# Performance work log

Measured on AMD Instinct MI355X. Metric: run time of the kernel, lower is better.

## Reference

```python
import jax, jax.numpy as jnp
import numpy as np

N_POINTS = 400000
N_SEG = 4096


def setup_inputs() -> dict:
    key = jax.random.key(0)
    ks = jax.random.split(key, 8)
    inp = {
        "features": jax.random.normal(ks[0], (N_POINTS, 11), dtype=jnp.float32),
        "super_indices": jax.random.randint(ks[1], (N_POINTS,), 0, N_SEG, dtype=jnp.int64) if jax.config.jax_enable_x64 else jax.random.randint(ks[1], (N_POINTS,), 0, N_SEG).astype(jnp.int32),
        "num_segments": N_SEG,
        "W1": jax.random.normal(ks[2], (11, 128), dtype=jnp.float32) * 0.02,
        "b1": jnp.zeros((128,), jnp.float32),
        "W2": jax.random.normal(ks[3], (128, 256), dtype=jnp.float32) * 0.02,
        "b2": jnp.zeros((256,), jnp.float32),
        "W3": jax.random.normal(ks[4], (512, 512), dtype=jnp.float32) * 0.02,
        "b3": jnp.zeros((512,), jnp.float32),
        "W4": jax.random.normal(ks[5], (512, 384), dtype=jnp.float32) * 0.02,
        "b4": jnp.zeros((384,), jnp.float32),
    }
    return inp


def reference(features, super_indices, num_segments, W1, b1, W2, b2, W3, b3, W4, b4):
    # first_conv: two 1x1 Conv1d == per-point linears (no activation between, as in source)
    h = features @ W1 + b1            # [N,128]
    h = h @ W2 + b2                   # [N,256]
    # per-superpoint global max (torch.max over group points)
    g = jax.ops.segment_max(h, super_indices, num_segments=num_segments)  # [S,256]
    # concat broadcasted group-global with local features -> 512 channels
    hcat = jnp.concatenate([g[super_indices], h], axis=-1)                # [N,512]
    # second_conv: Conv1d(512,512,1) -> ReLU -> Conv1d(512,token_embed_dim,1)
    z = jax.nn.relu(hcat @ W3 + b3)   # [N,512]
    z = z @ W4 + b4                   # [N,384]
    # final per-superpoint max pool -> one token per superpoint
    sp_features = jax.ops.segment_max(z, super_indices, num_segments=num_segments)  # [S,384]
    return sp_features
```

## Files before the change

### kernel.cpp

```cpp
#include <hip/hip_runtime.h>
#include <stdint.h>

#define GAS __attribute__((address_space(1)))
#define LAS __attribute__((address_space(3)))

typedef unsigned short u16;
typedef short short8 __attribute__((ext_vector_type(8)));
typedef __bf16 bf16x8 __attribute__((ext_vector_type(8)));
typedef float floatx4 __attribute__((ext_vector_type(4)));

__device__ __forceinline__ u16 f2bf(float f) {
  uint32_t u = __builtin_bit_cast(uint32_t, f);
  u += 0x7FFFu + ((u >> 16) & 1u);
  return (u16)(u >> 16);
}
__device__ __forceinline__ float bf2f(u16 h) {
  return __builtin_bit_cast(float, (uint32_t)h << 16);
}
__device__ __forceinline__ void split_bf(float v, u16& hi, u16& lo) {
  hi = f2bf(v);
  float r = v - bf2f(hi);
  if (!(r == r)) r = 0.f;
  lo = f2bf(r);
}

__device__ __forceinline__ void atomicMaxF(float* addr, float val) {
  if (!(val > *(volatile const float*)addr)) return;
  if (val >= 0.f) atomicMax((int*)addr, __builtin_bit_cast(int, val));
  else            atomicMin((unsigned int*)addr, __builtin_bit_cast(unsigned int, val));
}

__device__ __forceinline__ void async16(const void* g, const void* lds) {
  __builtin_amdgcn_global_load_lds((GAS const uint32_t*)g, (LAS uint32_t*)lds, 16, 0, 0);
}

__device__ __forceinline__ floatx4 mfma_bf16(short8 a, short8 b, floatx4 c) {
  return __builtin_amdgcn_mfma_f32_16x16x32_bf16(
      __builtin_bit_cast(bf16x8, a), __builtin_bit_cast(bf16x8, b), c, 0, 0, 0);
}

__global__ void k_init(float* __restrict__ g, float* __restrict__ out,
                       int* __restrict__ hist, int ng, int no, int nh) {
  int i = blockIdx.x * 256 + threadIdx.x;
  if (i < ng) g[i] = -INFINITY;
  else if (i < ng + no) out[i - ng] = -INFINITY;
  else if (i < ng + no + nh) hist[i - ng - no] = 0;
}

__global__ void k_hist(const int* __restrict__ idx, int* __restrict__ hist, int n) {
  int p = blockIdx.x * 256 + threadIdx.x;
  if (p < n) atomicAdd(&hist[idx[p]], 1);
}

__global__ __launch_bounds__(1024) void k_scan(const int* __restrict__ hist,
                                               int* __restrict__ offs, int* __restrict__ cur) {
  __shared__ int buf[2][1024];
  int t = threadIdx.x;
  int local[4];
  int s = 0;
#pragma unroll
  for (int j = 0; j < 4; ++j) { local[j] = hist[t * 4 + j]; s += local[j]; }
  buf[0][t] = s;
  __syncthreads();
  int pb = 0;
  for (int d = 1; d < 1024; d <<= 1) {
    int v = buf[pb][t] + (t >= d ? buf[pb][t - d] : 0);
    buf[pb ^ 1][t] = v;
    pb ^= 1;
    __syncthreads();
  }
  int run = (t == 0) ? 0 : buf[pb][t - 1];
#pragma unroll
  for (int j = 0; j < 4; ++j) { offs[t * 4 + j] = run; cur[t * 4 + j] = run; run += local[j]; }
}

__global__ void k_scatter(const int* __restrict__ idx, int* __restrict__ cur,
                          int* __restrict__ perm, int* __restrict__ segp, int n) {
  int p = blockIdx.x * 256 + threadIdx.x;
  if (p >= n) return;
  int s = idx[p];
  int r = atomicAdd(&cur[s], 1);
  perm[r] = p;
  segp[r] = s;
}

__global__ void k_h1(const float* __restrict__ feat, const int* __restrict__ perm,
                     const float* __restrict__ W1, const float* __restrict__ b1,
                     u16* __restrict__ h1hi, u16* __restrict__ h1lo,
                     int pt_off, int npts_chunk) {
  int gid = blockIdx.x * 256 + threadIdx.x;
  int p = gid >> 7, c = gid & 127;
  if (p >= npts_chunk) return;
  int o = perm[pt_off + p];
  float v = b1[c];
#pragma unroll
  for (int j = 0; j < 11; ++j) v += feat[o * 11 + j] * W1[j * 128 + c];
  u16 hi, lo; split_bf(v, hi, lo);
  h1hi[gid] = hi; h1lo[gid] = lo;
}

__global__ void k_wprep(const float* __restrict__ W, u16* __restrict__ bt, int K, int N) {
  int gid = blockIdx.x * 256 + threadIdx.x;
  if (gid >= K * N) return;
  int c = gid / K, k = gid - c * K;
  float v = W[(size_t)k * N + c];
  u16 hi, lo; split_bf(v, hi, lo);
  size_t b = (size_t)c * (3 * K);
  bt[b + k] = hi; bt[b + K + k] = lo; bt[b + 2 * K + k] = hi;
}

__global__ void k_w23(const float* __restrict__ W2, const float* __restrict__ W3,
                      const float* __restrict__ b2, const float* __restrict__ b3,
                      float* __restrict__ W23, float* __restrict__ b23) {
  int gid = blockIdx.x * 256 + threadIdx.x;
  if (gid < 128 * 512) {
    int j = gid >> 9, c = gid & 511;
    float s = 0.f;
#pragma unroll 4
    for (int t = 0; t < 256; ++t) s += W2[j * 256 + t] * W3[(size_t)(256 + t) * 512 + c];
    W23[gid] = s;
  } else if (gid < 128 * 512 + 512) {
    int c = gid - 128 * 512;
    float s = b3[c];
    for (int t = 0; t < 256; ++t) s += b2[t] * W3[(size_t)(256 + t) * 512 + c];
    b23[c] = s;
  }
}

__global__ void k_prep3(const float* __restrict__ W3, const float* __restrict__ W23,
                        u16* __restrict__ bt) {
  int gid = blockIdx.x * 256 + threadIdx.x;
  if (gid >= 512 * 384) return;
  int c = gid / 384, k = gid - c * 384;
  float v = (k < 256) ? W3[(size_t)k * 512 + c] : W23[(size_t)(k - 256) * 512 + c];
  u16 hi, lo; split_bf(v, hi, lo);
  size_t b = (size_t)c * 1152;
  bt[b + k] = hi; bt[b + 384 + k] = lo; bt[b + 768 + k] = hi;
}

__global__ void k_gsplit(const float* __restrict__ g, u16* __restrict__ ghi,
                         u16* __restrict__ glo, int n) {
  int i = blockIdx.x * 256 + threadIdx.x;
  if (i >= n) return;
  u16 hi, lo; split_bf(g[i], hi, lo);
  ghi[i] = hi; glo[i] = lo;
}

template <int MODE, int KP, int NT, int CW>
__global__ __launch_bounds__(256) void k_gemm(
    const u16* __restrict__ a0, const u16* __restrict__ a1,
    const u16* __restrict__ a2, const u16* __restrict__ a3,
    const u16* __restrict__ bt, const float* __restrict__ bias,
    const int* __restrict__ segp, int mt0,
    float* __restrict__ gmax, u16* __restrict__ whi, u16* __restrict__ wlo) {
  __shared__ __align__(16) union {
    struct { u16 A[128 * 64]; u16 B[128 * 64]; } st;
    float ct[128 * 66];
  } sm;
  const int tid = threadIdx.x;
  const int w = tid >> 6, lane = tid & 63;
  const int mtl = blockIdx.x / NT, ct = blockIdx.x % NT;
  const int wr = w & 1, wc = w >> 1;
  const int l15 = lane & 15, l4 = lane >> 4;
  const int sub = lane >> 3;
  const int kc8 = (lane & 7) * 8;

  int arl[4], bcol[4], gq[4];
#pragma unroll
  for (int q = 0; q < 4; ++q) {
    int rr = (q * 4 + w) * 8 + sub;
    arl[q] = mtl * 128 + rr;
    bcol[q] = ct * 128 + rr;
    if constexpr (MODE == 1) gq[q] = segp[(mt0 + mtl) * 128 + rr];
  }

  floatx4 zero = {0.f, 0.f, 0.f, 0.f};
  floatx4 acc[4][4];
#pragma unroll
  for (int mi = 0; mi < 4; ++mi)
#pragma unroll
    for (int ni = 0; ni < 4; ++ni) acc[mi][ni] = zero;

  for (int kt = 0; kt < KP / 64; ++kt) {
    const int kbase = kt * 64 + kc8;
#pragma unroll
    for (int q = 0; q < 4; ++q) {
      const u16* src;
      if constexpr (MODE == 0) {
        int r = kbase >> 7, k = kbase & 127;
        src = ((r == 2) ? a1 : a0) + (size_t)arl[q] * 128 + k;
      } else if constexpr (MODE == 1) {
        int r = kbase / 384, inner = kbase - r * 384;
        bool lo = (r == 2);
        if (inner < 256) src = (lo ? a2 : a0) + (size_t)gq[q] * 256 + inner;
        else             src = (lo ? a3 : a1) + (size_t)arl[q] * 128 + (inner - 256);
      } else {
        int r = kbase >> 9, inner = kbase & 511;
        src = ((r == 2) ? a1 : a0) + (size_t)arl[q] * 512 + inner;
      }
      async16(src, &sm.st.A[(q * 4 + w) * 512]);
    }
#pragma unroll
    for (int q = 0; q < 4; ++q)
      async16(bt + (size_t)bcol[q] * KP + kbase, &sm.st.B[(q * 4 + w) * 512]);
    __syncthreads();
#pragma unroll
    for (int kk = 0; kk < 2; ++kk) {
      short8 af[4], bfr[4];
#pragma unroll
      for (int mi = 0; mi < 4; ++mi)
        af[mi] = *(const short8*)&sm.st.A[(wr * 64 + mi * 16 + l15) * 64 + kk * 32 + l4 * 8];
#pragma unroll
      for (int ni = 0; ni < 4; ++ni)
        bfr[ni] = *(const short8*)&sm.st.B[(wc * 64 + ni * 16 + l15) * 64 + kk * 32 + l4 * 8];
#pragma unroll
      for (int mi = 0; mi < 4; ++mi)
#pragma unroll
        for (int ni = 0; ni < 4; ++ni)
          acc[mi][ni] = mfma_bf16(af[mi], bfr[ni], acc[mi][ni]);
    }
    __syncthreads();
  }

  if constexpr (MODE == 1) {
#pragma unroll
    for (int ni = 0; ni < 4; ++ni) {
      const int col = ct * 128 + wc * 64 + ni * 16 + l15;
      const float bv = bias[col];
#pragma unroll
      for (int mi = 0; mi < 4; ++mi) {
        const int rl0 = mtl * 128 + wr * 64 + mi * 16 + l4 * 4;
#pragma unroll
        for (int r = 0; r < 4; ++r) {
          float v = fmaxf(acc[mi][ni][r] + bv, 0.f);
          u16 hi, lo; split_bf(v, hi, lo);
          whi[(size_t)(rl0 + r) * 512 + col] = hi;
          wlo[(size_t)(rl0 + r) * 512 + col] = lo;
        }
      }
    }
  } else {
#pragma unroll
    for (int h = 0; h < 2; ++h) {
      __syncthreads();
      if (wc == h) {
#pragma unroll
        for (int ni = 0; ni < 4; ++ni) {
          const int cl = ni * 16 + l15;
          const float bv = bias[ct * 128 + h * 64 + cl];
#pragma unroll
          for (int mi = 0; mi < 4; ++mi) {
            const int row0 = wr * 64 + mi * 16 + l4 * 4;
#pragma unroll
            for (int r = 0; r < 4; ++r)
              sm.ct[(row0 + r) * 66 + cl] = acc[mi][ni][r] + bv;
          }
        }
      }
      __syncthreads();
      if (tid < 128) {
        const int col = tid & 63, rh = tid >> 6;
        const int cg = ct * 128 + h * 64 + col;
        const int base = (mt0 + mtl) * 128 + rh * 64;
        float run = sm.ct[(rh * 64) * 66 + col];
        int curs = segp[base];
        for (int r = 1; r < 64; ++r) {
          int s = segp[base + r];
          float v = sm.ct[(rh * 64 + r) * 66 + col];
          if (s != curs) {
            atomicMaxF(&gmax[(size_t)curs * CW + cg], run);
            run = v; curs = s;
          } else {
            run = fmaxf(run, v);
          }
        }
        atomicMaxF(&gmax[(size_t)curs * CW + cg], run);
      }
    }
  }
}

extern "C" void kernel_launch(void* const* d_in, const int* in_sizes, int n_in,
                              void* d_out, int out_size, void* d_ws, size_t ws_size,
                              hipStream_t stream) {
  const float* feat = (const float*)d_in[0];
  const int* sidx   = (const int*)d_in[1];
  const float* W1 = (const float*)d_in[3];
  const float* b1 = (const float*)d_in[4];
  const float* W2 = (const float*)d_in[5];
  const float* b2 = (const float*)d_in[6];
  const float* W3 = (const float*)d_in[7];
  const float* b3 = (const float*)d_in[8];
  const float* W4 = (const float*)d_in[9];
  const float* b4 = (const float*)d_in[10];
  float* out = (float*)d_out;
  (void)n_in;

  const int S  = out_size / 384;
  const int NP = in_sizes[1];
  const int MT = NP / 128;

  char* ws = (char*)d_ws;
  size_t off = 0;
  auto carve = [&](size_t bytes) -> void* {
    void* p = ws + off;
    off += (bytes + 255) & ~(size_t)255;
    return p;
  };
  float* g   = (float*)carve((size_t)S * 256 * 4);
  u16* ghi   = (u16*)carve((size_t)S * 256 * 2);
  u16* glo   = (u16*)carve((size_t)S * 256 * 2);
  u16* B2t   = (u16*)carve((size_t)256 * 384 * 2);
  u16* B3t   = (u16*)carve((size_t)512 * 1152 * 2);
  u16* B4t   = (u16*)carve((size_t)384 * 1536 * 2);
  float* W23 = (float*)carve((size_t)128 * 512 * 4);
  float* b23 = (float*)carve((size_t)512 * 4);
  int* hist  = (int*)carve((size_t)S * 4);
  int* offs  = (int*)carve((size_t)S * 4);
  int* curp  = (int*)carve((size_t)S * 4);
  int* perm  = (int*)carve((size_t)NP * 4);
  int* segp  = (int*)carve((size_t)NP * 4);

  const size_t per_block = (size_t)128 * (128 * 2 * 2 + 512 * 2 * 2) + 4 * 256;
  size_t remain = (ws_size > off + 4096) ? (ws_size - off - 4096) : 0;
  int cb = (int)(remain / per_block);
  if (cb < 1) cb = 1;
  if (cb > MT) cb = MT;
  u16* h1hi = (u16*)carve((size_t)cb * 128 * 128 * 2);
  u16* h1lo = (u16*)carve((size_t)cb * 128 * 128 * 2);
  u16* z1hi = (u16*)carve((size_t)cb * 128 * 512 * 2);
  u16* z1lo = (u16*)carve((size_t)cb * 128 * 512 * 2);

  k_init<<<(S * (256 + 384 + 1) + 255) / 256, 256, 0, stream>>>(g, out, hist,
                                                                S * 256, S * 384, S);
  k_hist<<<(NP + 255) / 256, 256, 0, stream>>>(sidx, hist, NP);
  k_scan<<<1, 1024, 0, stream>>>(hist, offs, curp);
  k_scatter<<<(NP + 255) / 256, 256, 0, stream>>>(sidx, curp, perm, segp, NP);

  k_wprep<<<(128 * 256 + 255) / 256, 256, 0, stream>>>(W2, B2t, 128, 256);
  k_w23<<<(128 * 512 + 512 + 255) / 256, 256, 0, stream>>>(W2, W3, b2, b3, W23, b23);
  k_prep3<<<(512 * 384 + 255) / 256, 256, 0, stream>>>(W3, W23, B3t);
  k_wprep<<<(512 * 384 + 255) / 256, 256, 0, stream>>>(W4, B4t, 512, 384);

  for (int done = 0; done < MT; done += cb) {
    int nb = (MT - done < cb) ? (MT - done) : cb;
    int pts = nb * 128;
    k_h1<<<(pts * 128) / 256, 256, 0, stream>>>(feat, perm, W1, b1, h1hi, h1lo,
                                                done * 128, pts);
    k_gemm<0, 384, 2, 256><<<nb * 2, 256, 0, stream>>>(
        h1hi, h1lo, nullptr, nullptr, B2t, b2, segp, done, g, nullptr, nullptr);
  }
  k_gsplit<<<(S * 256 + 255) / 256, 256, 0, stream>>>(g, ghi, glo, S * 256);

  for (int done = 0; done < MT; done += cb) {
    int nb = (MT - done < cb) ? (MT - done) : cb;
    int pts = nb * 128;
    k_h1<<<(pts * 128) / 256, 256, 0, stream>>>(feat, perm, W1, b1, h1hi, h1lo,
                                                done * 128, pts);
    k_gemm<1, 1152, 4, 0><<<nb * 4, 256, 0, stream>>>(
        ghi, h1hi, glo, h1lo, B3t, b23, segp, done, nullptr, z1hi, z1lo);
    k_gemm<2, 1536, 3, 384><<<nb * 3, 256, 0, stream>>>(
        z1hi, z1lo, nullptr, nullptr, B4t, b4, segp, done, out, nullptr, nullptr);
  }
}
```

Measured before the change: 3.058 ms.

## Double-buffer GEMM LDS tiles and remap blocks across XCDs

The GEMM kernel now stages A/B tiles into two LDS buffers, issuing async loads for the next K-step before computing the current one, so global latency overlaps with MFMA work. It also remaps block IDs so contiguous work items land on the same XCD, improving L2 reuse of weight and activation tiles. LDS use doubles, which may reduce occupancy, and padded grids add a few idle blocks.

```diff
diff --git a/kernel.cpp b/kernel.cpp
--- a/kernel.cpp
+++ b/kernel.cpp
@@ -151,15 +151,21 @@
     const u16* __restrict__ a0, const u16* __restrict__ a1,
     const u16* __restrict__ a2, const u16* __restrict__ a3,
     const u16* __restrict__ bt, const float* __restrict__ bias,
-    const int* __restrict__ segp, int mt0,
+    const int* __restrict__ segp, int mt0, int nb,
     float* __restrict__ gmax, u16* __restrict__ whi, u16* __restrict__ wlo) {
   __shared__ __align__(16) union {
-    struct { u16 A[128 * 64]; u16 B[128 * 64]; } st;
+    struct { u16 A[2][128 * 64]; u16 B[2][128 * 64]; } st;
     float ct[128 * 66];
   } sm;
   const int tid = threadIdx.x;
   const int w = tid >> 6, lane = tid & 63;
-  const int mtl = blockIdx.x / NT, ct = blockIdx.x % NT;
+
+  const int work_total = nb * NT;
+  const int spx = (work_total + 7) >> 3;
+  const int wk = (blockIdx.x & 7) * spx + (blockIdx.x >> 3);
+  if (wk >= work_total) return;
+  const int mtl = wk / NT, ct = wk - mtl * NT;
+
   const int wr = w & 1, wc = w >> 1;
   const int l15 = lane & 15, l4 = lane >> 4;
   const int sub = lane >> 3;
@@ -174,14 +180,7 @@
     if constexpr (MODE == 1) gq[q] = segp[(mt0 + mtl) * 128 + rr];
   }
 
-  floatx4 zero = {0.f, 0.f, 0.f, 0.f};
-  floatx4 acc[4][4];
-#pragma unroll
-  for (int mi = 0; mi < 4; ++mi)
-#pragma unroll
-    for (int ni = 0; ni < 4; ++ni) acc[mi][ni] = zero;
-
-  for (int kt = 0; kt < KP / 64; ++kt) {
+  auto stage = [&](int kt, int buf) {
     const int kbase = kt * 64 + kc8;
 #pragma unroll
     for (int q = 0; q < 4; ++q) {
@@ -198,21 +197,35 @@
         int r = kbase >> 9, inner = kbase & 511;
         src = ((r == 2) ? a1 : a0) + (size_t)arl[q] * 512 + inner;
       }
-      async16(src, &sm.st.A[(q * 4 + w) * 512]);
+      async16(src, &sm.st.A[buf][(q * 4 + w) * 512]);
     }
 #pragma unroll
     for (int q = 0; q < 4; ++q)
-      async16(bt + (size_t)bcol[q] * KP + kbase, &sm.st.B[(q * 4 + w) * 512]);
-    __syncthreads();
+      async16(bt + (size_t)bcol[q] * KP + kbase, &sm.st.B[buf][(q * 4 + w) * 512]);
+  };
+
+  floatx4 zero = {0.f, 0.f, 0.f, 0.f};
+  floatx4 acc[4][4];
+#pragma unroll
+  for (int mi = 0; mi < 4; ++mi)
+#pragma unroll
+    for (int ni = 0; ni < 4; ++ni) acc[mi][ni] = zero;
+
+  constexpr int NKT = KP / 64;
+  stage(0, 0);
+  __syncthreads();
+  int cur = 0;
+  for (int kt = 0; kt < NKT; ++kt) {
+    if (kt + 1 < NKT) stage(kt + 1, cur ^ 1);
 #pragma unroll
     for (int kk = 0; kk < 2; ++kk) {
       short8 af[4], bfr[4];
 #pragma unroll
       for (int mi = 0; mi < 4; ++mi)
-        af[mi] = *(const short8*)&sm.st.A[(wr * 64 + mi * 16 + l15) * 64 + kk * 32 + l4 * 8];
+        af[mi] = *(const short8*)&sm.st.A[cur][(wr * 64 + mi * 16 + l15) * 64 + kk * 32 + l4 * 8];
 #pragma unroll
       for (int ni = 0; ni < 4; ++ni)
-        bfr[ni] = *(const short8*)&sm.st.B[(wc * 64 + ni * 16 + l15) * 64 + kk * 32 + l4 * 8];
+        bfr[ni] = *(const short8*)&sm.st.B[cur][(wc * 64 + ni * 16 + l15) * 64 + kk * 32 + l4 * 8];
 #pragma unroll
       for (int mi = 0; mi < 4; ++mi)
 #pragma unroll
@@ -220,6 +233,7 @@
           acc[mi][ni] = mfma_bf16(af[mi], bfr[ni], acc[mi][ni]);
     }
     __syncthreads();
+    cur ^= 1;
   }
 
   if constexpr (MODE == 1) {
@@ -280,6 +294,8 @@
   }
 }
 
+static inline int swgrid(int work) { return 8 * ((work + 7) / 8); }
+
 extern "C" void kernel_launch(void* const* d_in, const int* in_sizes, int n_in,
                               void* d_out, int out_size, void* d_ws, size_t ws_size,
                               hipStream_t stream) {
@@ -347,8 +363,8 @@
     int pts = nb * 128;
     k_h1<<<(pts * 128) / 256, 256, 0, stream>>>(feat, perm, W1, b1, h1hi, h1lo,
                                                 done * 128, pts);
-    k_gemm<0, 384, 2, 256><<<nb * 2, 256, 0, stream>>>(
-        h1hi, h1lo, nullptr, nullptr, B2t, b2, segp, done, g, nullptr, nullptr);
+    k_gemm<0, 384, 2, 256><<<swgrid(nb * 2), 256, 0, stream>>>(
+        h1hi, h1lo, nullptr, nullptr, B2t, b2, segp, done, nb, g, nullptr, nullptr);
   }
   k_gsplit<<<(S * 256 + 255) / 256, 256, 0, stream>>>(g, ghi, glo, S * 256);
 
@@ -357,9 +373,9 @@
     int pts = nb * 128;
     k_h1<<<(pts * 128) / 256, 256, 0, stream>>>(feat, perm, W1, b1, h1hi, h1lo,
                                                 done * 128, pts);
-    k_gemm<1, 1152, 4, 0><<<nb * 4, 256, 0, stream>>>(
-        ghi, h1hi, glo, h1lo, B3t, b23, segp, done, nullptr, z1hi, z1lo);
-    k_gemm<2, 1536, 3, 384><<<nb * 3, 256, 0, stream>>>(
-        z1hi, z1lo, nullptr, nullptr, B4t, b4, segp, done, out, nullptr, nullptr);
-  }
-}
+    k_gemm<1, 1152, 4, 0><<<swgrid(nb * 4), 256, 0, stream>>>(
+        ghi, h1hi, glo, h1lo, B3t, b23, segp, done, nb, nullptr, z1hi, z1lo);
+    k_gemm<2, 1536, 3, 384><<<swgrid(nb * 3), 256, 0, stream>>>(
+        z1hi, z1lo, nullptr, nullptr, B4t, b4, segp, done, nb, out, nullptr, nullptr);
+  }
+}
```

After: 2.637 ms. 1.16x faster.
